# Kernel optimization log

Measured on AMD Instinct MI355X. Metric: run time of the kernel, lower is better.

The kernel has to match this reference:

```python
import jax, jax.numpy as jnp
import numpy as np

HIDDEN = 1024
HEADS = 16
HEAD_DIM = HIDDEN // HEADS


def setup_inputs() -> dict:
    key = jax.random.key(0)
    k0, k1, k2, k3, k4 = jax.random.split(key, 5)
    s = 0.02
    return {
        "data": jax.random.normal(k0, (4, 2048, HIDDEN), dtype=jnp.float32),
        "qkv_w": jax.random.normal(k1, (3 * HIDDEN, HIDDEN), dtype=jnp.float32) * s,  # (out,in) torch layout
        "qkv_b": jax.random.normal(k2, (3 * HIDDEN,), dtype=jnp.float32) * s,
        "out_w": jax.random.normal(k3, (HIDDEN, HIDDEN), dtype=jnp.float32) * s,
        "out_b": jax.random.normal(k4, (HIDDEN,), dtype=jnp.float32) * s,
    }


def reference(data, qkv_w, qkv_b, out_w, out_b):
    B, T, C = data.shape
    qkv = jnp.einsum("btc,oc->bto", data, qkv_w) + qkv_b  # [B,T,3C]
    q, k, v = jnp.split(qkv, 3, axis=2)
    # [B,T,C] -> [B,H,T,D]
    def heads(x):
        return x.reshape(B, T, HEADS, HEAD_DIM).transpose(0, 2, 1, 3)
    q, k, v = heads(q), heads(k), heads(v)
    scale = 1.0 / jnp.sqrt(jnp.float32(HEAD_DIM))
    att = jnp.einsum("bhqd,bhkd->bhqk", q, k) * scale  # [B,H,T,T]
    causal = jnp.tril(jnp.ones((T, T), dtype=bool))
    att = jnp.where(causal[None, None, :, :], att, -jnp.inf)
    att = jax.nn.softmax(att, axis=-1)
    out = jnp.einsum("bhqk,bhkd->bhqd", att, v)  # [B,H,T,D]
    out = out.transpose(0, 2, 1, 3).reshape(B, T, C)
    return jnp.einsum("btc,oc->bto", out, out_w) + out_b
```

## Files before the change

kernel.cpp:

```cpp
#include <hip/hip_runtime.h>
#include <hip/hip_bf16.h>
#include <stdint.h>

typedef __attribute__((ext_vector_type(8))) __bf16 bf16x8;
typedef __attribute__((ext_vector_type(4))) float f32x4;
typedef __attribute__((ext_vector_type(16))) float f32x16;
typedef __attribute__((ext_vector_type(4))) unsigned int u32x4;

#define HIDDEN 1024
#define HEADS 16
#define HD 64
#define NB 4
#define T_ 2048
#define M_ROWS (NB * T_)
#define SCL2 0.18033688f
#define FIXM 32.0f

__device__ __forceinline__ unsigned short f2bf(float x) {
  unsigned u = __builtin_bit_cast(unsigned, x);
  u += 0x7fff + ((u >> 16) & 1);
  return (unsigned short)(u >> 16);
}

__device__ __forceinline__ unsigned pk2(float a, float b) {
  unsigned ua = __builtin_bit_cast(unsigned, a) + 0x8000u;
  unsigned ub = __builtin_bit_cast(unsigned, b) + 0x8000u;
  return __builtin_amdgcn_perm(ub, ua, 0x07060302);
}

__device__ __forceinline__ f32x4 mfma16(bf16x8 a, bf16x8 b, f32x4 c) {
  return __builtin_amdgcn_mfma_f32_16x16x32_bf16(a, b, c, 0, 0, 0);
}
__device__ __forceinline__ f32x16 mfma32(bf16x8 a, bf16x8 b, f32x16 c) {
  return __builtin_amdgcn_mfma_f32_32x32x16_bf16(a, b, c, 0, 0, 0);
}

__device__ __forceinline__ void lds16(const void* g, void* l) {
  __builtin_amdgcn_global_load_lds(
      (const __attribute__((address_space(1))) unsigned int*)g,
      (__attribute__((address_space(3))) unsigned int*)l, 16, 0, 0);
}

__device__ __forceinline__ bf16x8 ldg8(const unsigned short* p) {
  return __builtin_bit_cast(bf16x8, *(const u32x4*)p);
}

__global__ void cvt_bf16(const float* __restrict__ in,
                         unsigned short* __restrict__ out, int n4) {
  int i = blockIdx.x * blockDim.x + threadIdx.x;
  int stride = gridDim.x * blockDim.x;
  for (; i < n4; i += stride) {
    float4 v = ((const float4*)in)[i];
    ushort4 o;
    o.x = f2bf(v.x); o.y = f2bf(v.y); o.z = f2bf(v.z); o.w = f2bf(v.w);
    ((ushort4*)out)[i] = o;
  }
}


#define RD(BUF, OFF) \
  __builtin_bit_cast(bf16x8, *(const u32x4*)((BUF) + (OFF)))

template <int EPI, int NT>
__global__ __launch_bounds__(512, 4) void gemm8(
    const unsigned short* __restrict__ A, const unsigned short* __restrict__ Bm,
    const float* __restrict__ bias, unsigned short* __restrict__ Qb,
    unsigned short* __restrict__ Kb, unsigned short* __restrict__ Vtb,
    float* __restrict__ Cf) {
  constexpr int K = 1024;
  constexpr int N = NT * 256;
  __shared__ __align__(16) char LB[3][24576];
  const int tid = threadIdx.x;
  const int wv = tid >> 6, lane = tid & 63;
  const int l16 = lane & 15, grp = lane >> 4;
  const int wm = wv >> 2, wn = wv & 3;
  const int bid = blockIdx.x;
  const int sw = (bid & 7) * ((64 * NT) >> 3) + (bid >> 3);
  const int by = sw / NT, bx = sw % NT;
  const int brow0 = by * 128, bcol0 = bx * 256;

  const int ua = (tid & 7) ^ ((tid >> 3) & 7);
  const unsigned short* aptr =
      A + (size_t)(brow0 + (tid >> 3) * 2 + (ua >> 2)) * K + (ua & 3) * 8;
  const unsigned short* bptr =
      Bm + (size_t)(bcol0 + (tid >> 3) * 2 + (ua >> 2)) * K + (ua & 3) * 8;

  const int swu = ((((l16 & 1) * 4) + grp) ^ ((l16 >> 1) & 7)) * 16;
  const int aoff = (wm * 32 + (l16 >> 1)) * 128 + swu;
  const int boff = 8192 + (wn * 32 + (l16 >> 1)) * 128 + swu;

#define STAGE(c, t)                                                   \
  do {                                                                \
    lds16(aptr + (size_t)(t) * 32, (char*)LB[c] + wv * 1024);         \
    lds16(bptr + (size_t)(t) * 32, (char*)LB[c] + 8192 + wv * 1024);  \
    lds16(bptr + (size_t)128 * K + (size_t)(t) * 32,                  \
          (char*)LB[c] + 16384 + wv * 1024);                          \
  } while (0)

  f32x4 acc[4][4];
#pragma unroll
  for (int m = 0; m < 4; m++)
#pragma unroll
    for (int n = 0; n < 4; n++) acc[m][n] = (f32x4){0.f, 0.f, 0.f, 0.f};

  STAGE(0, 0);
  STAGE(1, 1);
  asm volatile("s_waitcnt vmcnt(3)" ::: "memory");
  __builtin_amdgcn_sched_barrier(0);
  __builtin_amdgcn_s_barrier();

  int c = 0, c2 = 2;
#pragma unroll 1
  for (int t = 0; t < 32; ++t) {
    const char* buf = (const char*)LB[c];
    bf16x8 bf[4], af[4];
#pragma unroll
    for (int n = 0; n < 4; n++) bf[n] = RD(buf, boff + n * 1024);
#pragma unroll
    for (int m = 0; m < 4; m++) af[m] = RD(buf, aoff + m * 1024);
    if (t < 30) STAGE(c2, t + 2);
    __builtin_amdgcn_s_barrier();
    __builtin_amdgcn_s_setprio(1);
#pragma unroll
    for (int m = 0; m < 4; m++)
#pragma unroll
      for (int n = 0; n < 4; n++) acc[m][n] = mfma16(af[m], bf[n], acc[m][n]);
    __builtin_amdgcn_s_setprio(0);
    if (t < 30) {
      asm volatile("s_waitcnt vmcnt(3)" ::: "memory");
      __builtin_amdgcn_sched_barrier(0);
    } else if (t == 30) {
      asm volatile("s_waitcnt vmcnt(0)" ::: "memory");
      __builtin_amdgcn_sched_barrier(0);
    }
    if (t < 31) __builtin_amdgcn_s_barrier();
    c = (c == 2) ? 0 : c + 1;
    c2 = (c2 == 2) ? 0 : c2 + 1;
  }

#pragma unroll
  for (int m = 0; m < 4; m++) {
#pragma unroll
    for (int n = 0; n < 4; n++) {
      int col = bcol0 + wn * 64 + n * 16 + l16;
      int row0 = brow0 + wm * 64 + m * 16 + grp * 4;
      float bs = bias[col];
      if (EPI == 0) {
        int part = col >> 10, rem = col & 1023;
        int h = rem >> 6, d = rem & 63;
#pragma unroll
        for (int r = 0; r < 4; r++) {
          int rw = row0 + r;
          int b = rw >> 11, t = rw & 2047;
          unsigned short val = f2bf(acc[m][n][r] + bs);
          size_t bh = (size_t)(b * 16 + h);
          if (part == 0)
            Qb[(bh * T_ + t) * HD + d] = val;
          else if (part == 1)
            Kb[(bh * T_ + t) * HD + d] = val;
          else {
            int k = t & 31;
            int rr = (k & 3) + 4 * (k >> 3);
            int s = (rr & 7) + 8 * ((k >> 2) & 1) + 16 * (rr >> 3);
            Vtb[(bh * HD + d) * T_ + (t & ~31) + s] = val;
          }
        }
      } else {
#pragma unroll
        for (int r = 0; r < 4; r++)
          Cf[(size_t)(row0 + r) * N + col] = acc[m][n][r] + bs;
      }
    }
  }
#undef STAGE
}

__global__ __launch_bounds__(256, 3) void attn32(
    const unsigned short* __restrict__ Q, const unsigned short* __restrict__ K,
    const unsigned short* __restrict__ Vt, unsigned short* __restrict__ Ao) {
  __shared__ __align__(16) unsigned short Kl[2][32 * 64];
  __shared__ __align__(16) unsigned short Vl[2][32 * 64];
  const int i = blockIdx.x;
  const int bh = i & 63;
  const int g = (i < 512) ? (15 - (i >> 6)) : ((i - 512) >> 6);
  const int wv = threadIdx.x >> 6, lane = threadIdx.x & 63;
  const int l31 = lane & 31, hi = lane >> 5;
  const int qt = g * 4 + wv;
  const int maxqt = g * 4 + 3;
  const unsigned short* Qh = Q + (size_t)bh * T_ * HD;
  const unsigned short* Kh = K + (size_t)bh * T_ * HD;
  const unsigned short* Vh = Vt + (size_t)bh * HD * T_;
  const int b_ = bh >> 4, h_ = bh & 15;

  const int sj = threadIdx.x >> 3, su = threadIdx.x & 7;
  const int sup = su ^ (sj & 7);
  const unsigned short* ksrc = Kh + sj * HD + sup * 8;
  const unsigned short* vsrc =
      Vh + (size_t)(sj + 32 * (sup >> 2)) * T_ + (sup & 3) * 8;
  char* kdst0 = (char*)&Kl[0][0] + wv * 1024;
  char* kdst1 = (char*)&Kl[1][0] + wv * 1024;
  char* vdst0 = (char*)&Vl[0][0] + wv * 1024;
  char* vdst1 = (char*)&Vl[1][0] + wv * 1024;

#define STAGE(B, KC)                                     \
  do {                                                   \
    int kt_ = (KC) * 32;                                 \
    lds16(ksrc + (size_t)kt_ * HD, (B) ? kdst1 : kdst0); \
    lds16(vsrc + kt_, (B) ? vdst1 : vdst0);              \
  } while (0)

  int rdoff[4];
#pragma unroll
  for (int ks = 0; ks < 4; ks++)
    rdoff[ks] = l31 * 128 + (((2 * ks + hi) ^ (l31 & 7)) << 4);

  bf16x8 qf[4];
  const int qbase = qt * 32;
#pragma unroll
  for (int st = 0; st < 4; st++)
    qf[st] = ldg8(&Qh[(size_t)(qbase + l31) * HD + st * 16 + hi * 8]);

  f32x16 o0, o1;
#pragma unroll
  for (int r = 0; r < 16; r++) { o0[r] = 0.f; o1[r] = 0.f; }
  float rl = 0.f;

#define CHUNK(B, MASKED)                                                     \
  do {                                                                       \
    const char* kb = (const char*)&Kl[(B)][0];                               \
    const char* vb = (const char*)&Vl[(B)][0];                               \
    bf16x8 KF[4], VF[4];                                                     \
    _Pragma("unroll") for (int ks = 0; ks < 4; ks++) {                       \
      KF[ks] = __builtin_bit_cast(bf16x8, *(const u32x4*)(kb + rdoff[ks]));  \
      VF[ks] = __builtin_bit_cast(bf16x8, *(const u32x4*)(vb + rdoff[ks]));  \
    }                                                                        \
    f32x16 sa;                                                               \
    _Pragma("unroll") for (int r = 0; r < 16; r++) sa[r] = 0.f;              \
    sa = mfma32(KF[0], qf[0], sa);                                           \
    sa = mfma32(KF[1], qf[1], sa);                                           \
    sa = mfma32(KF[2], qf[2], sa);                                           \
    sa = mfma32(KF[3], qf[3], sa);                                           \
    float pv[16];                                                            \
    _Pragma("unroll") for (int r = 0; r < 16; r++) {                         \
      float arg = __builtin_fmaf(sa[r], SCL2, -FIXM);                        \
      if (MASKED) {                                                          \
        int key = (r & 3) + 8 * (r >> 2) + 4 * hi;                           \
        if (key > l31) arg = -1e30f;                                         \
      }                                                                      \
      pv[r] = exp2f(arg);                                                    \
      rl += pv[r];                                                           \
    }                                                                        \
    u32x4 pa0u, pa1u;                                                        \
    pa0u.x = pk2(pv[0], pv[1]);                                              \
    pa0u.y = pk2(pv[2], pv[3]);                                              \
    pa0u.z = pk2(pv[4], pv[5]);                                              \
    pa0u.w = pk2(pv[6], pv[7]);                                              \
    pa1u.x = pk2(pv[8], pv[9]);                                              \
    pa1u.y = pk2(pv[10], pv[11]);                                            \
    pa1u.z = pk2(pv[12], pv[13]);                                            \
    pa1u.w = pk2(pv[14], pv[15]);                                            \
    bf16x8 pa0 = __builtin_bit_cast(bf16x8, pa0u);                           \
    bf16x8 pa1 = __builtin_bit_cast(bf16x8, pa1u);                           \
    o0 = mfma32(VF[0], pa0, o0);                                             \
    o0 = mfma32(VF[1], pa1, o0);                                             \
    o1 = mfma32(VF[2], pa0, o1);                                             \
    o1 = mfma32(VF[3], pa1, o1);                                             \
  } while (0)

  STAGE(0, 0);
  __syncthreads();
  int cur = 0;
  for (int kc = 0; kc <= maxqt; kc++) {
    if (kc < maxqt) STAGE(cur ^ 1, kc + 1);
    if (kc < qt) {
      CHUNK(cur, 0);
    } else if (kc == qt) {
      CHUNK(cur, 1);
    }
    __syncthreads();
    cur ^= 1;
  }

  float rlt = rl + __shfl_xor(rl, 32);
  float inv = 1.f / rlt;
  const size_t base =
      ((size_t)b_ * T_ + qbase + l31) * HIDDEN + h_ * HD + hi * 4;
#pragma unroll
  for (int gg = 0; gg < 4; gg++) {
    uint2 u;
    u.x = pk2(o0[4 * gg] * inv, o0[4 * gg + 1] * inv);
    u.y = pk2(o0[4 * gg + 2] * inv, o0[4 * gg + 3] * inv);
    *(uint2*)&Ao[base + gg * 8] = u;
  }
#pragma unroll
  for (int gg = 0; gg < 4; gg++) {
    uint2 u;
    u.x = pk2(o1[4 * gg] * inv, o1[4 * gg + 1] * inv);
    u.y = pk2(o1[4 * gg + 2] * inv, o1[4 * gg + 3] * inv);
    *(uint2*)&Ao[base + 32 + gg * 8] = u;
  }
#undef STAGE
#undef CHUNK
}

extern "C" void kernel_launch(void* const* d_in, const int* in_sizes, int n_in,
                              void* d_out, int out_size, void* d_ws,
                              size_t ws_size, hipStream_t stream) {
  const float* data = (const float*)d_in[0];
  const float* qkvw = (const float*)d_in[1];
  const float* qkvb = (const float*)d_in[2];
  const float* outw = (const float*)d_in[3];
  const float* outb = (const float*)d_in[4];
  float* out = (float*)d_out;
  char* ws = (char*)d_ws;

  unsigned short* dataBf = (unsigned short*)(ws);
  unsigned short* qkvwBf = (unsigned short*)(ws + 16777216);
  unsigned short* outwBf = (unsigned short*)(ws + 23068672);
  unsigned short* Qb = (unsigned short*)(ws + 25165824);
  unsigned short* Kb = (unsigned short*)(ws + 41943040);
  unsigned short* Vtb = (unsigned short*)(ws + 58720256);
  unsigned short* attnO = dataBf;

  cvt_bf16<<<2048, 256, 0, stream>>>(data, dataBf, (M_ROWS * HIDDEN) / 4);
  cvt_bf16<<<1024, 256, 0, stream>>>(qkvw, qkvwBf, (3 * HIDDEN * HIDDEN) / 4);
  cvt_bf16<<<512, 256, 0, stream>>>(outw, outwBf, (HIDDEN * HIDDEN) / 4);

  gemm8<0, 12><<<768, 512, 0, stream>>>(dataBf, qkvwBf, qkvb, Qb, Kb, Vtb,
                                        nullptr);
  attn32<<<1024, 256, 0, stream>>>(Qb, Kb, Vtb, attnO);
  gemm8<1, 4><<<256, 512, 0, stream>>>(attnO, outwBf, outb, nullptr, nullptr,
                                       nullptr, out);
}
```

Measured before the change: 198.3 us.

## Enlarge GEMM tiles to 256x256 with K=64 double-buffered phased pipeline

After: 202.3 us. No clear change (+2.0%).

```diff
diff --git a/kernel.cpp b/kernel.cpp
--- a/kernel.cpp
+++ b/kernel.cpp
@@ -62,117 +62,143 @@
   __builtin_bit_cast(bf16x8, *(const u32x4*)((BUF) + (OFF)))
 
 template <int EPI, int NT>
-__global__ __launch_bounds__(512, 4) void gemm8(
+__global__ __launch_bounds__(512, 2) void gemm256(
     const unsigned short* __restrict__ A, const unsigned short* __restrict__ Bm,
     const float* __restrict__ bias, unsigned short* __restrict__ Qb,
     unsigned short* __restrict__ Kb, unsigned short* __restrict__ Vtb,
     float* __restrict__ Cf) {
   constexpr int K = 1024;
   constexpr int N = NT * 256;
-  __shared__ __align__(16) char LB[3][24576];
+  __shared__ __align__(16) char LB[131072];
   const int tid = threadIdx.x;
   const int wv = tid >> 6, lane = tid & 63;
   const int l16 = lane & 15, grp = lane >> 4;
   const int wm = wv >> 2, wn = wv & 3;
   const int bid = blockIdx.x;
-  const int sw = (bid & 7) * ((64 * NT) >> 3) + (bid >> 3);
+  const int sw = (bid & 7) * (4 * NT) + (bid >> 3);
   const int by = sw / NT, bx = sw % NT;
-  const int brow0 = by * 128, bcol0 = bx * 256;
-
-  const int ua = (tid & 7) ^ ((tid >> 3) & 7);
-  const unsigned short* aptr =
-      A + (size_t)(brow0 + (tid >> 3) * 2 + (ua >> 2)) * K + (ua & 3) * 8;
-  const unsigned short* bptr =
-      Bm + (size_t)(bcol0 + (tid >> 3) * 2 + (ua >> 2)) * K + (ua & 3) * 8;
-
-  const int swu = ((((l16 & 1) * 4) + grp) ^ ((l16 >> 1) & 7)) * 16;
-  const int aoff = (wm * 32 + (l16 >> 1)) * 128 + swu;
-  const int boff = 8192 + (wn * 32 + (l16 >> 1)) * 128 + swu;
-
-#define STAGE(c, t)                                                   \
-  do {                                                                \
-    lds16(aptr + (size_t)(t) * 32, (char*)LB[c] + wv * 1024);         \
-    lds16(bptr + (size_t)(t) * 32, (char*)LB[c] + 8192 + wv * 1024);  \
-    lds16(bptr + (size_t)128 * K + (size_t)(t) * 32,                  \
-          (char*)LB[c] + 16384 + wv * 1024);                          \
+  const int brow0 = by * 256, bcol0 = bx * 256;
+
+  const int trow = tid >> 3;
+  const int ua = (tid & 7) ^ (trow & 7);
+  const unsigned short* aSrc = A + (size_t)(brow0 + trow) * K + ua * 8;
+  const unsigned short* bSrc = Bm + (size_t)(bcol0 + trow) * K + ua * 8;
+
+#define SA(b, h, t)                                                         \
+  do {                                                                      \
+    lds16(aSrc + (size_t)((h) * 128) * K + (t) * 64,                        \
+          LB + (b) * 65536 + (h) * 16384 + wv * 1024);                      \
+    lds16(aSrc + (size_t)((h) * 128 + 64) * K + (t) * 64,                   \
+          LB + (b) * 65536 + (h) * 16384 + 8192 + wv * 1024);               \
   } while (0)
-
-  f32x4 acc[4][4];
-#pragma unroll
-  for (int m = 0; m < 4; m++)
+#define SB(b, h, t)                                                         \
+  do {                                                                      \
+    lds16(bSrc + (size_t)((h) * 128) * K + (t) * 64,                        \
+          LB + (b) * 65536 + 32768 + (h) * 16384 + wv * 1024);              \
+    lds16(bSrc + (size_t)((h) * 128 + 64) * K + (t) * 64,                   \
+          LB + (b) * 65536 + 32768 + (h) * 16384 + 8192 + wv * 1024);       \
+  } while (0)
+
+  const int rsw = l16 & 7;
+  const int sw0 = (grp ^ rsw) << 4;
+  const int sw1 = ((4 + grp) ^ rsw) << 4;
+  const int aBase0 = wm * 16384 + l16 * 128;
+  const int bBase0 = 32768 + wn * 8192 + l16 * 128;
+
+  f32x4 acc[8][4];
+#pragma unroll
+  for (int m = 0; m < 8; m++)
 #pragma unroll
     for (int n = 0; n < 4; n++) acc[m][n] = (f32x4){0.f, 0.f, 0.f, 0.f};
-
-  STAGE(0, 0);
-  STAGE(1, 1);
-  asm volatile("s_waitcnt vmcnt(3)" ::: "memory");
+  bf16x8 bfr[4];
+
+#define PHASE(BUF, MS, KK, READB, STAGES, WAITS)                             \
+  {                                                                          \
+    if (READB) {                                                             \
+      _Pragma("unroll") for (int n = 0; n < 4; n++) bfr[n] =                 \
+          RD(LB, (BUF) + bBase0 + n * 2048 + ((KK) ? sw1 : sw0));            \
+    }                                                                        \
+    bf16x8 af[4];                                                            \
+    _Pragma("unroll") for (int m = 0; m < 4; m++) af[m] =                    \
+        RD(LB, (BUF) + aBase0 + (MS) * 8192 + m * 2048 + ((KK) ? sw1 : sw0));\
+    STAGES;                                                                  \
+    __builtin_amdgcn_s_barrier();                                            \
+    __builtin_amdgcn_s_setprio(1);                                           \
+    _Pragma("unroll") for (int m = 0; m < 4; m++)                            \
+        _Pragma("unroll") for (int n = 0; n < 4; n++) acc[(MS) * 4 + m][n] = \
+            mfma16(af[m], bfr[n], acc[(MS) * 4 + m][n]);                     \
+    __builtin_amdgcn_s_setprio(0);                                           \
+    WAITS;                                                                   \
+    __builtin_amdgcn_s_barrier();                                            \
+  }
+
+  SA(0, 0, 0); SA(0, 1, 0); SB(0, 0, 0); SB(0, 1, 0);
+  SB(1, 0, 1); SB(1, 1, 1);
+  asm volatile("s_waitcnt vmcnt(4)" ::: "memory");
   __builtin_amdgcn_sched_barrier(0);
   __builtin_amdgcn_s_barrier();
 
-  int c = 0, c2 = 2;
 #pragma unroll 1
-  for (int t = 0; t < 32; ++t) {
-    const char* buf = (const char*)LB[c];
-    bf16x8 bf[4], af[4];
-#pragma unroll
-    for (int n = 0; n < 4; n++) bf[n] = RD(buf, boff + n * 1024);
-#pragma unroll
-    for (int m = 0; m < 4; m++) af[m] = RD(buf, aoff + m * 1024);
-    if (t < 30) STAGE(c2, t + 2);
-    __builtin_amdgcn_s_barrier();
-    __builtin_amdgcn_s_setprio(1);
-#pragma unroll
-    for (int m = 0; m < 4; m++)
-#pragma unroll
-      for (int n = 0; n < 4; n++) acc[m][n] = mfma16(af[m], bf[n], acc[m][n]);
-    __builtin_amdgcn_s_setprio(0);
-    if (t < 30) {
-      asm volatile("s_waitcnt vmcnt(3)" ::: "memory");
-      __builtin_amdgcn_sched_barrier(0);
-    } else if (t == 30) {
-      asm volatile("s_waitcnt vmcnt(0)" ::: "memory");
-      __builtin_amdgcn_sched_barrier(0);
-    }
-    if (t < 31) __builtin_amdgcn_s_barrier();
-    c = (c == 2) ? 0 : c + 1;
-    c2 = (c2 == 2) ? 0 : c2 + 1;
-  }
-
-#pragma unroll
-  for (int m = 0; m < 4; m++) {
-#pragma unroll
-    for (int n = 0; n < 4; n++) {
-      int col = bcol0 + wn * 64 + n * 16 + l16;
-      int row0 = brow0 + wm * 64 + m * 16 + grp * 4;
-      float bs = bias[col];
-      if (EPI == 0) {
-        int part = col >> 10, rem = col & 1023;
-        int h = rem >> 6, d = rem & 63;
-#pragma unroll
-        for (int r = 0; r < 4; r++) {
-          int rw = row0 + r;
-          int b = rw >> 11, t = rw & 2047;
-          unsigned short val = f2bf(acc[m][n][r] + bs);
-          size_t bh = (size_t)(b * 16 + h);
-          if (part == 0)
-            Qb[(bh * T_ + t) * HD + d] = val;
-          else if (part == 1)
-            Kb[(bh * T_ + t) * HD + d] = val;
-          else {
-            int k = t & 31;
-            int rr = (k & 3) + 4 * (k >> 3);
-            int s = (rr & 7) + 8 * ((k >> 2) & 1) + 16 * (rr >> 3);
-            Vtb[(bh * HD + d) * T_ + (t & ~31) + s] = val;
+  for (int i = 0; i < 8; ++i) {
+    const int t = 2 * i;
+    const bool more = (i < 7);
+    PHASE(0, 0, 0, 1, { SA(1, 0, t + 1); }, {});
+    PHASE(0, 1, 0, 0, { SA(1, 1, t + 1); }, {});
+    PHASE(0, 0, 1, 1, {}, {});
+    PHASE(0, 1, 1, 0,
+          { if (more) { SB(0, 0, t + 2); SB(0, 1, t + 2); } },
+          { if (more) { asm volatile("s_waitcnt vmcnt(4)" ::: "memory"); }
+            else      { asm volatile("s_waitcnt vmcnt(0)" ::: "memory"); }
+            __builtin_amdgcn_sched_barrier(0); });
+    PHASE(65536, 0, 0, 1, { if (more) SA(0, 0, t + 2); }, {});
+    PHASE(65536, 1, 0, 0, { if (more) SA(0, 1, t + 2); }, {});
+    PHASE(65536, 0, 1, 1, {}, {});
+    PHASE(65536, 1, 1, 0,
+          { if (more) { SB(1, 0, t + 3); SB(1, 1, t + 3); } },
+          { if (more) { asm volatile("s_waitcnt vmcnt(4)" ::: "memory");
+                        __builtin_amdgcn_sched_barrier(0); } });
+  }
+
+#pragma unroll
+  for (int ms = 0; ms < 2; ms++) {
+#pragma unroll
+    for (int m = 0; m < 4; m++) {
+#pragma unroll
+      for (int n = 0; n < 4; n++) {
+        int col = bcol0 + wn * 64 + n * 16 + l16;
+        int row0 = brow0 + wm * 128 + ms * 64 + m * 16 + grp * 4;
+        float bs = bias[col];
+        if (EPI == 0) {
+          int part = col >> 10, rem = col & 1023;
+          int h = rem >> 6, d = rem & 63;
+#pragma unroll
+          for (int r = 0; r < 4; r++) {
+            int rw = row0 + r;
+            int b = rw >> 11, t2 = rw & 2047;
+            unsigned short val = f2bf(acc[ms * 4 + m][n][r] + bs);
+            size_t bh = (size_t)(b * 16 + h);
+            if (part == 0)
+              Qb[(bh * T_ + t2) * HD + d] = val;
+            else if (part == 1)
+              Kb[(bh * T_ + t2) * HD + d] = val;
+            else {
+              int k = t2 & 31;
+              int rr = (k & 3) + 4 * (k >> 3);
+              int s = (rr & 7) + 8 * ((k >> 2) & 1) + 16 * (rr >> 3);
+              Vtb[(bh * HD + d) * T_ + (t2 & ~31) + s] = val;
+            }
           }
+        } else {
+#pragma unroll
+          for (int r = 0; r < 4; r++)
+            Cf[(size_t)(row0 + r) * N + col] = acc[ms * 4 + m][n][r] + bs;
         }
-      } else {
-#pragma unroll
-        for (int r = 0; r < 4; r++)
-          Cf[(size_t)(row0 + r) * N + col] = acc[m][n][r] + bs;
       }
     }
   }
-#undef STAGE
+#undef SA
+#undef SB
+#undef PHASE
 }
 
 __global__ __launch_bounds__(256, 3) void attn32(
@@ -326,9 +352,9 @@
   cvt_bf16<<<1024, 256, 0, stream>>>(qkvw, qkvwBf, (3 * HIDDEN * HIDDEN) / 4);
   cvt_bf16<<<512, 256, 0, stream>>>(outw, outwBf, (HIDDEN * HIDDEN) / 4);
 
-  gemm8<0, 12><<<768, 512, 0, stream>>>(dataBf, qkvwBf, qkvb, Qb, Kb, Vtb,
-                                        nullptr);
+  gemm256<0, 12><<<384, 512, 0, stream>>>(dataBf, qkvwBf, qkvb, Qb, Kb, Vtb,
+                                          nullptr);
   attn32<<<1024, 256, 0, stream>>>(Qb, Kb, Vtb, attnO);
-  gemm8<1, 4><<<256, 512, 0, stream>>>(attnO, outwBf, outb, nullptr, nullptr,
-                                       nullptr, out);
-}
+  gemm256<1, 4><<<128, 512, 0, stream>>>(attnO, outwBf, outb, nullptr, nullptr,
+                                         nullptr, out);
+}
```
